# Performance work log

Measured on AMD Instinct MI355X. Metric: run time of the kernel, lower is better.

Reference implementation:

```python
import jax, jax.numpy as jnp
import numpy as np

B, T, F, H, D = 64, 256, 128, 8, 256
E = F * H          # MHA embed dim = input_dim * feat_dim = 1024
HEADS = 4
HD = E // HEADS


def setup_inputs() -> dict:
    key = jax.random.key(0)
    ks = jax.random.split(key, 12)
    def w(k, shape, fan_in):
        return (jax.random.normal(k, shape, jnp.float32) / np.float32(np.sqrt(fan_in)))
    z = lambda *s: jnp.zeros(s, jnp.float32)
    return {
        "x": jax.random.normal(ks[0], (B, T, F), jnp.float32),
        # input_attn MLP: Linear(F, F//4) -> GELU -> Linear(F//4, F) -> Sigmoid
        "attn_w1": w(ks[1], (F, F // 4), F), "attn_b1": z(F // 4),
        "attn_w2": w(ks[2], (F // 4, F), F // 4), "attn_b2": z(F),
        # bank of F tiny GRUs (input=1, hidden=H), stacked along feature axis
        "W_ih": w(ks[3], (F, 3 * H), 1),        # input weight per feature (input size 1)
        "W_hh": w(ks[4], (F, 3 * H, H), H),
        "b_ih": z(F, 3 * H), "b_hh": z(F, 3 * H),
        # MultiheadAttention(E, 4 heads)
        "in_proj_w": w(ks[5], (E, 3 * E), E), "in_proj_b": z(3 * E),
        "mha_out_w": w(ks[6], (E, E), E), "mha_out_b": z(E),
        # out_proj: Linear(E, D)
        "outp_w": w(ks[7], (E, D), E), "outp_b": z(D),
        # FFN: Linear(D, 2D) -> GELU -> Linear(2D, D)
        "ffn_w1": w(ks[8], (D, 2 * D), D), "ffn_b1": z(2 * D),
        "ffn_w2": w(ks[9], (2 * D, D), 2 * D), "ffn_b2": z(D),
    }


def _forward(x, attn_w1, attn_b1, attn_w2, attn_b2,
             W_ih, W_hh, b_ih, b_hh,
             in_proj_w, in_proj_b, mha_out_w, mha_out_b,
             outp_w, outp_b, ffn_w1, ffn_b1, ffn_w2, ffn_b2):
    gelu = lambda v: jax.nn.gelu(v, approximate=False)
    bs, ts, _ = x.shape
    # feature gating (dropout layers are identity in eval mode)
    input_attn = jax.nn.sigmoid(gelu(x @ attn_w1 + attn_b1) @ attn_w2 + attn_b2)  # [B,T,F]
    xg = x * input_attn

    # fused bank of F independent GRUs (input size 1, hidden H), scanned over time
    def step(h, xt):  # h: [B,F,H], xt: [B,F]
        gi = xt[..., None] * W_ih + b_ih                       # [B,F,3H]
        gh = jnp.einsum('bfh,fgh->bfg', h, W_hh) + b_hh        # [B,F,3H]
        ir, iz, inn = jnp.split(gi, 3, axis=-1)
        hr, hz, hn = jnp.split(gh, 3, axis=-1)
        r = jax.nn.sigmoid(ir + hr)
        zg = jax.nn.sigmoid(iz + hz)
        n = jnp.tanh(inn + r * hn)
        h_new = (1.0 - zg) * n + zg * h
        return h_new, h_new

    h0 = jnp.zeros((bs, F, H), x.dtype)
    _, ys = jax.lax.scan(step, h0, jnp.moveaxis(xg, 1, 0))     # ys: [T,B,F,H]
    out = jnp.moveaxis(ys, 0, 1).reshape(bs, ts, E)            # [B,T,E]

    # self-attention (eval: no dropout)
    qkv = out @ in_proj_w + in_proj_b                          # [B,T,3E]
    q, k, v = jnp.split(qkv, 3, axis=-1)
    hsplit = lambda t: t.reshape(bs, ts, HEADS, HD)
    q, k, v = hsplit(q), hsplit(k), hsplit(v)
    scores = jnp.einsum('bqhd,bkhd->bhqk', q, k) / np.float32(np.sqrt(HD))
    attn = jax.nn.softmax(scores, axis=-1)
    ctx = jnp.einsum('bhqk,bkhd->bqhd', attn, v).reshape(bs, ts, E)
    mha_out = ctx @ mha_out_w + mha_out_b

    h1 = mha_out @ outp_w + outp_b                             # [B,T,D]
    ffn = gelu(h1 @ ffn_w1 + ffn_b1) @ ffn_w2 + ffn_b2
    y = h1 + ffn
    feature_importance = input_attn.sum(-1)                    # [B,T]
    return y, feature_importance, input_attn


def reference(x, attn_w1, attn_b1, attn_w2, attn_b2,
              W_ih, W_hh, b_ih, b_hh,
              in_proj_w, in_proj_b, mha_out_w, mha_out_b,
              outp_w, outp_b, ffn_w1, ffn_b1, ffn_w2, ffn_b2):
    return _forward(x, attn_w1, attn_b1, attn_w2, attn_b2,
                    W_ih, W_hh, b_ih, b_hh,
                    in_proj_w, in_proj_b, mha_out_w, mha_out_b,
                    outp_w, outp_b, ffn_w1, ffn_b1, ffn_w2, ffn_b2)
```

## Files before the change

kernel.cpp:

```cpp
#include <hip/hip_runtime.h>
#include <hip/hip_bf16.h>
#include <math.h>

#define B_  64
#define T_  256
#define F_  128
#define H_  8
#define E_  1024
#define NH_ 4
#define HD_ 256
#define D_  256

#define OFF_Y_  0L
#define OFF_FI_ 4194304L
#define OFF_IA_ 4210688L

typedef unsigned short u16;
typedef unsigned int   u32;
typedef short bf16x8 __attribute__((ext_vector_type(8)));
typedef float f32x4  __attribute__((ext_vector_type(4)));

__device__ __forceinline__ float bf2f(u16 u) {
  union { u32 u; float f; } x; x.u = ((u32)u) << 16; return x.f;
}
__device__ __forceinline__ u16 f2bf(float f) {
  union { float f; u32 u; } x; x.f = f;
  u32 r = (x.u + 0x7fffu + ((x.u >> 16) & 1u)) >> 16;
  return (u16)r;
}
__device__ __forceinline__ float gelu_exact(float v) {
  return 0.5f * v * (1.f + erff(v * 0.70710678118654752f));
}
__device__ __forceinline__ float sigmoidf_(float v) {
  return 1.f / (1.f + __expf(-v));
}
__device__ __forceinline__ float ldv(const void* p, long i, bool isf) {
  return isf ? ((const float*)p)[i] : bf2f(((const u16*)p)[i]);
}
__device__ __forceinline__ void stv(void* p, long i, float v, bool isf) {
  if (isf) ((float*)p)[i] = v;
  else ((u16*)p)[i] = f2bf(v);
}
__device__ __forceinline__ void gld16(void* lds, const void* g) {
  __builtin_amdgcn_global_load_lds(
      (const __attribute__((address_space(1))) u32*)g,
      (__attribute__((address_space(3))) u32*)lds, 16, 0, 0);
}
#define MFMA_ __builtin_amdgcn_mfma_f32_16x16x32_bf16

__global__ void detect_dtype(const u16* __restrict__ x, u32* __restrict__ flag) {
  if (threadIdx.x == 0 && blockIdx.x == 0) {
    int good = 0;
    for (int i = 0; i < 512; ++i) {
      u16 v = x[i];
      int e = (v >> 7) & 0xFF;
      if (v == 0 || (e >= 100 && e <= 140)) ++good;
    }
    *flag = (good >= 450) ? 0u : 1u;
  }
}

__device__ __forceinline__ void do_transpose(const void* __restrict__ in,
                                             u16* __restrict__ out, int R, int C,
                                             int bx, int by, bool isf,
                                             float (*t)[33], int tid) {
  const int tx = tid & 31, ty0 = tid >> 5;
  const int c0 = bx * 32, r0 = by * 32;
  for (int i = ty0; i < 32; i += 8)
    t[i][tx] = ldv(in, (long)(r0 + i) * C + c0 + tx, isf);
  __syncthreads();
  for (int i = ty0; i < 32; i += 8)
    out[(long)(c0 + i) * R + r0 + tx] = f2bf(t[tx][i]);
}

__global__ __launch_bounds__(256)
void uberprep(const void* __restrict__ x,
              const void* __restrict__ w1, const void* __restrict__ b1,
              const void* __restrict__ w2, const void* __restrict__ b2,
              const void* __restrict__ ipw, const void* __restrict__ mhw,
              const void* __restrict__ opw, const void* __restrict__ f1w,
              const void* __restrict__ f2w,
              const void* __restrict__ ipb, const void* __restrict__ mhb,
              const void* __restrict__ opb, const void* __restrict__ f1b,
              const void* __restrict__ f2b,
              const u32* __restrict__ flag,
              u16* __restrict__ xg,
              u16* __restrict__ wtI, u16* __restrict__ wtM, u16* __restrict__ wtO,
              u16* __restrict__ wtF1, u16* __restrict__ wtF2,
              u16* __restrict__ biasa, void* __restrict__ dout) {
  const bool isf = (*flag != 0);
  const int bid = blockIdx.x;
  const int tid = threadIdx.x;
  __shared__ float xr[2][F_];
  __shared__ float hid4[2][4][32];
  __shared__ float hid[2][32];
  __shared__ float red[4];
  __shared__ float tt[32][33];
  if (bid < 8192) {
    const int sub = tid >> 7, t7 = tid & 127;
    const long row = (long)bid * 2 + sub;
    float xv = ldv(x, row * F_ + t7, isf);
    xr[sub][t7] = xv;
    __syncthreads();
    {
      const int g = t7 & 31, part = t7 >> 5;
      const int f0 = part * 32;
      float s = 0.f;
      #pragma unroll 8
      for (int f = 0; f < 32; ++f)
        s += xr[sub][f0 + f] * ldv(w1, (long)(f0 + f) * 32 + g, isf);
      hid4[sub][part][g] = s;
    }
    __syncthreads();
    if (t7 < 32)
      hid[sub][t7] = gelu_exact(ldv(b1, t7, isf) + hid4[sub][0][t7] + hid4[sub][1][t7]
                                + hid4[sub][2][t7] + hid4[sub][3][t7]);
    __syncthreads();
    float s = ldv(b2, t7, isf);
    #pragma unroll 8
    for (int j = 0; j < 32; ++j) s += hid[sub][j] * ldv(w2, j * F_ + t7, isf);
    float ia = sigmoidf_(s);
    stv(dout, OFF_IA_ + row * F_ + t7, ia, isf);
    xg[row * F_ + t7] = f2bf(ia * xv);
    float v = ia;
    for (int o = 32; o > 0; o >>= 1) v += __shfl_down(v, o);
    if ((tid & 63) == 0) red[tid >> 6] = v;
    __syncthreads();
    if (t7 == 0) stv(dout, OFF_FI_ + row, red[sub * 2] + red[sub * 2 + 1], isf);
  } else if (bid < 11264) {
    const int r = bid - 8192;
    do_transpose(ipw, wtI, 1024, 3072, r % 96, r / 96, isf, tt, tid);
  } else if (bid < 12288) {
    const int r = bid - 11264;
    do_transpose(mhw, wtM, 1024, 1024, r % 32, r / 32, isf, tt, tid);
  } else if (bid < 12544) {
    const int r = bid - 12288;
    do_transpose(opw, wtO, 1024, 256, r % 8, r / 8, isf, tt, tid);
  } else if (bid < 12672) {
    const int r = bid - 12544;
    do_transpose(f1w, wtF1, 256, 512, r % 16, r / 16, isf, tt, tid);
  } else if (bid < 12800) {
    const int r = bid - 12672;
    do_transpose(f2w, wtF2, 512, 256, r % 8, r / 8, isf, tt, tid);
  } else {
    const int i = (bid - 12800) * 256 + tid;
    if (i < 5120) {
      const void* s; long off;
      if (i < 3072)      { s = ipb; off = i; }
      else if (i < 4096) { s = mhb; off = i - 3072; }
      else if (i < 4352) { s = opb; off = i - 4096; }
      else if (i < 4864) { s = f1b; off = i - 4352; }
      else               { s = f2b; off = i - 4864; }
      biasa[i] = f2bf(ldv(s, off, isf));
    }
  }
}

__global__ __launch_bounds__(256)
void gru_scan4(const u16* __restrict__ xg, const void* __restrict__ W_ih,
               const void* __restrict__ W_hh, const void* __restrict__ b_ih,
               const void* __restrict__ b_hh, const u32* __restrict__ flag,
               u16* __restrict__ gruo) {
  const bool isf = (*flag != 0);
  const int tid = threadIdx.x;
  const int ric = tid >> 3;
  const int j   = tid & 7;
  const int rec = blockIdx.x * 32 + ric;
  const int b = rec >> 7, f = rec & 127;
  __shared__ __align__(16) float hbuf[32][8];
  float whr[8], whz[8], whn[8];
  #pragma unroll
  for (int k = 0; k < 8; ++k) {
    whr[k] = ldv(W_hh, (long)f * 192 + j * 8 + k, isf);
    whz[k] = ldv(W_hh, (long)f * 192 + (8 + j) * 8 + k, isf);
    whn[k] = ldv(W_hh, (long)f * 192 + (16 + j) * 8 + k, isf);
  }
  const float wir = ldv(W_ih, f * 24 + j, isf);
  const float wiz = ldv(W_ih, f * 24 + 8 + j, isf);
  const float win = ldv(W_ih, f * 24 + 16 + j, isf);
  const float cbr = ldv(b_ih, f * 24 + j, isf) + ldv(b_hh, f * 24 + j, isf);
  const float cbz = ldv(b_ih, f * 24 + 8 + j, isf) + ldv(b_hh, f * 24 + 8 + j, isf);
  const float bin_ = ldv(b_ih, f * 24 + 16 + j, isf);
  const float bhn_ = ldv(b_hh, f * 24 + 16 + j, isf);
  float h[8];
  #pragma unroll
  for (int k = 0; k < 8; ++k) h[k] = 0.f;
  const u16* xp = xg + (long)b * T_ * F_ + f;
  u16* op = gruo + (long)b * T_ * E_ + f * 8 + j;
  float xv = bf2f(xp[0]);
  for (int t = 0; t < T_; ++t) {
    float xn = (t + 1 < T_) ? bf2f(xp[(t + 1) * F_]) : 0.f;
    float ar = fmaf(xv, wir, cbr);
    float az = fmaf(xv, wiz, cbz);
    float an = bhn_;
    #pragma unroll
    for (int k = 0; k < 8; ++k) {
      ar = fmaf(h[k], whr[k], ar);
      az = fmaf(h[k], whz[k], az);
      an = fmaf(h[k], whn[k], an);
    }
    const float r = sigmoidf_(ar);
    const float z = sigmoidf_(az);
    const float a = fmaf(r, an, fmaf(xv, win, bin_));
    const float e = __expf(2.f * a);
    const float n = 1.f - 2.f / (e + 1.f);
    const float hn = fmaf(z, h[j] - n, n);
    op[(long)t * E_] = f2bf(hn);
    hbuf[ric][j] = hn;
    f32x4 h0 = *(const f32x4*)&hbuf[ric][0];
    f32x4 h1 = *(const f32x4*)&hbuf[ric][4];
    h[0] = h0[0]; h[1] = h0[1]; h[2] = h0[2]; h[3] = h0[3];
    h[4] = h1[0]; h[5] = h1[1]; h[6] = h1[2]; h[7] = h1[3];
    xv = xn;
  }
}

template <int EPI>
__global__ __launch_bounds__(256)
void gemm_bt(const u16* __restrict__ A, int lda,
             const u16* __restrict__ Bp, int ldb,
             u16* __restrict__ Cg, int ldc,
             const u16* __restrict__ bias,
             int K, int nbm) {
  const int bm = blockIdx.x % nbm, bn = blockIdx.x / nbm;
  const int w = threadIdx.x >> 6, lane = threadIdx.x & 63;
  __shared__ __align__(16) u16 As[128 * 64];
  __shared__ __align__(16) u16 Bs[128 * 64];
  const long m0 = (long)bm * 128, n0 = (long)bn * 128;
  const int wm = w >> 1, wn = w & 1;
  const int lr8 = lane >> 3;
  const int csw = ((lane & 7) ^ (lr8 & 7)) * 8;
  f32x4 acc[4][4] = {};
  const int nk = K >> 6;
  const int lr = lane & 15, lq = lane >> 4;
  for (int kt = 0; kt < nk; ++kt) {
    const int k0 = kt << 6;
    __syncthreads();
    #pragma unroll
    for (int c = 0; c < 4; ++c) {
      const int rb = w * 32 + c * 8;
      gld16((char*)As + rb * 128, A + (m0 + rb + lr8) * (long)lda + k0 + csw);
      gld16((char*)Bs + rb * 128, Bp + (n0 + rb + lr8) * (long)ldb + k0 + csw);
    }
    __syncthreads();
    #pragma unroll
    for (int sub = 0; sub < 2; ++sub) {
      const int ch = sub * 4 + lq;
      const int cof = ((ch ^ (lr & 7)) << 3);
      bf16x8 af[4], bfv[4];
      #pragma unroll
      for (int i = 0; i < 4; ++i)
        af[i] = *(const bf16x8*)&As[(wm * 64 + i * 16 + lr) * 64 + cof];
      #pragma unroll
      for (int i = 0; i < 4; ++i)
        bfv[i] = *(const bf16x8*)&Bs[(wn * 64 + i * 16 + lr) * 64 + cof];
      #pragma unroll
      for (int i = 0; i < 4; ++i) {
        #pragma unroll
        for (int j = 0; j < 4; ++j)
          acc[i][j] = MFMA_(af[i], bfv[j], acc[i][j], 0, 0, 0);
      }
    }
  }
  const int rq = lq * 4;
  #pragma unroll
  for (int j = 0; j < 4; ++j) {
    const long col = n0 + wn * 64 + j * 16 + lr;
    const float bv = (EPI >= 1) ? bf2f(bias[col]) : 0.f;
    #pragma unroll
    for (int i = 0; i < 4; ++i) {
      const long row0 = m0 + wm * 64 + i * 16 + rq;
      #pragma unroll
      for (int q = 0; q < 4; ++q)
        Cg[(row0 + q) * (long)ldc + col] = f2bf(acc[i][j][q] + bv);
    }
  }
}

__global__ __launch_bounds__(256)
void attn_fused(const u16* __restrict__ qkv, u16* __restrict__ ctx) {
  const int z = blockIdx.y, bb = z >> 2, hh = z & 3;
  const int w = threadIdx.x >> 6, lane = threadIdx.x & 63;
  const int tid = threadIdx.x;
  const long t0 = (long)blockIdx.x * 64;
  __shared__ __align__(16) u16 P1[10240];
  __shared__ __align__(16) u16 Pl[64 * 264];
  __shared__ __align__(16) u16 Vt[256 * 40];
  const u16* qb = qkv + (long)bb * T_ * 3 * E_ + hh * HD_;
  const u16* kb = qb + E_;
  const u16* vb = qb + 2 * E_;
  const int rr = lane >> 2, cc = lane & 3;
  const int lr = lane & 15, lq = lane >> 4, lk = lq * 8;
  f32x4 acc[16] = {};
  for (int kt = 0; kt < 8; ++kt) {
    const int k0 = kt * 32;
    __syncthreads();
    gld16((char*)P1 + w * 16 * 64, qb + (t0 + w * 16 + rr) * (3L * E_) + k0 + cc * 8);
    #pragma unroll
    for (int c = 0; c < 4; ++c) {
      const int rb = w * 64 + c * 16;
      gld16((char*)P1 + 4096 + rb * 64, kb + (long)(rb + rr) * (3L * E_) + k0 + cc * 8);
    }
    __syncthreads();
    bf16x8 aq = *(const bf16x8*)&P1[(w * 16 + lr) * 32 + lk];
    #pragma unroll
    for (int nt = 0; nt < 16; ++nt) {
      bf16x8 bk = *(const bf16x8*)&P1[2048 + (nt * 16 + lr) * 32 + lk];
      acc[nt] = MFMA_(aq, bk, acc[nt], 0, 0, 0);
    }
  }
  #pragma unroll
  for (int q = 0; q < 4; ++q) {
    float mx = -3.4e38f;
    #pragma unroll
    for (int nt = 0; nt < 16; ++nt) mx = fmaxf(mx, acc[nt][q]);
    mx = fmaxf(mx, __shfl_xor(mx, 1));
    mx = fmaxf(mx, __shfl_xor(mx, 2));
    mx = fmaxf(mx, __shfl_xor(mx, 4));
    mx = fmaxf(mx, __shfl_xor(mx, 8));
    float e[16], sum = 0.f;
    #pragma unroll
    for (int nt = 0; nt < 16; ++nt) {
      e[nt] = __expf((acc[nt][q] - mx) * 0.0625f);
      sum += e[nt];
    }
    sum += __shfl_xor(sum, 1);
    sum += __shfl_xor(sum, 2);
    sum += __shfl_xor(sum, 4);
    sum += __shfl_xor(sum, 8);
    const float inv = 1.f / sum;
    const int rowl = w * 16 + lq * 4 + q;
    #pragma unroll
    for (int nt = 0; nt < 16; ++nt)
      Pl[rowl * 264 + nt * 16 + lr] = f2bf(e[nt] * inv);
  }
  f32x4 acc2[16] = {};
  for (int st = 0; st < 8; ++st) {
    const int s0 = st * 32;
    __syncthreads();
    #pragma unroll
    for (int c = 0; c < 4; ++c) {
      const int rb = w * 8 + c * 2;
      gld16((char*)P1 + rb * 512, vb + (s0 + rb + (lane >> 5)) * (3L * E_) + (lane & 31) * 8);
    }
    __syncthreads();
    u16 col[32];
    #pragma unroll
    for (int si = 0; si < 32; ++si) col[si] = P1[si * 256 + tid];
    #pragma unroll
    for (int cq = 0; cq < 4; ++cq)
      *(uint4*)&Vt[tid * 40 + cq * 8] = *(const uint4*)&col[cq * 8];
    __syncthreads();
    bf16x8 pa = *(const bf16x8*)&Pl[(w * 16 + lr) * 264 + s0 + lk];
    #pragma unroll
    for (int nt = 0; nt < 16; ++nt) {
      bf16x8 bv = *(const bf16x8*)&Vt[(nt * 16 + lr) * 40 + lk];
      acc2[nt] = MFMA_(pa, bv, acc2[nt], 0, 0, 0);
    }
  }
  const int rq = lq * 4;
  #pragma unroll
  for (int nt = 0; nt < 16; ++nt) {
    const int cold = nt * 16 + lr;
    #pragma unroll
    for (int q = 0; q < 4; ++q) {
      const long row = t0 + w * 16 + rq + q;
      ctx[((long)bb * T_ + row) * E_ + hh * HD_ + cold] = f2bf(acc2[nt][q]);
    }
  }
}

__global__ __launch_bounds__(256)
void fused_tail(const u16* __restrict__ MHA,
                const u16* __restrict__ wtO, const u16* __restrict__ wtF1,
                const u16* __restrict__ wtF2,
                const u16* __restrict__ bO, const u16* __restrict__ bF1,
                const u16* __restrict__ bF2,
                void* __restrict__ Y, const u32* __restrict__ flag) {
  const bool isf = (*flag != 0);
  const int w = threadIdx.x >> 6, lane = threadIdx.x & 63;
  const long m0 = (long)blockIdx.x * 32;
  __shared__ __align__(16) u16 Astg[32 * 64];
  __shared__ __align__(16) u16 h1s[32 * 264];
  __shared__ __align__(16) u16 ffhs[32 * 520];
  const int lr = lane & 15, lq = lane >> 4;
  const int rq = lq * 4;
  const int srow = w * 8 + (lane >> 3);
  const int csw = ((lane & 7) ^ ((lane >> 3) & 7)) * 8;
  f32x4 acc1[2][4] = {};
  for (int kt = 0; kt < 16; ++kt) {
    const int k0 = kt << 6;
    __syncthreads();
    gld16(&Astg[w * 512], MHA + (m0 + srow) * 1024L + k0 + csw);
    __syncthreads();
    #pragma unroll
    for (int kk = 0; kk < 2; ++kk) {
      const int ch = kk * 4 + lq;
      const int cof = ((ch ^ (lr & 7)) << 3);
      bf16x8 af[2];
      #pragma unroll
      for (int i = 0; i < 2; ++i)
        af[i] = *(const bf16x8*)&Astg[(i * 16 + lr) * 64 + cof];
      #pragma unroll
      for (int j = 0; j < 4; ++j) {
        const int n = w * 64 + j * 16 + lr;
        bf16x8 bfv = *(const bf16x8*)(wtO + n * 1024L + k0 + kk * 32 + lq * 8);
        #pragma unroll
        for (int i = 0; i < 2; ++i)
          acc1[i][j] = MFMA_(af[i], bfv, acc1[i][j], 0, 0, 0);
      }
    }
  }
  __syncthreads();
  #pragma unroll
  for (int j = 0; j < 4; ++j) {
    const int col = w * 64 + j * 16 + lr;
    const float bv = bf2f(bO[col]);
    #pragma unroll
    for (int i = 0; i < 2; ++i)
      #pragma unroll
      for (int q = 0; q < 4; ++q)
        h1s[(i * 16 + rq + q) * 264 + col] = f2bf(acc1[i][j][q] + bv);
  }
  __syncthreads();
  f32x4 acc2[2][8] = {};
  for (int kt = 0; kt < 8; ++kt) {
    const int k0 = kt << 5;
    bf16x8 af[2];
    #pragma unroll
    for (int i = 0; i < 2; ++i)
      af[i] = *(const bf16x8*)&h1s[(i * 16 + lr) * 264 + k0 + lq * 8];
    #pragma unroll
    for (int j = 0; j < 8; ++j) {
      const int n = w * 128 + j * 16 + lr;
      bf16x8 bfv = *(const bf16x8*)(wtF1 + n * 256L + k0 + lq * 8);
      #pragma unroll
      for (int i = 0; i < 2; ++i)
        acc2[i][j] = MFMA_(af[i], bfv, acc2[i][j], 0, 0, 0);
    }
  }
  __syncthreads();
  #pragma unroll
  for (int j = 0; j < 8; ++j) {
    const int col = w * 128 + j * 16 + lr;
    const float bv = bf2f(bF1[col]);
    #pragma unroll
    for (int i = 0; i < 2; ++i)
      #pragma unroll
      for (int q = 0; q < 4; ++q)
        ffhs[(i * 16 + rq + q) * 520 + col] = f2bf(gelu_exact(acc2[i][j][q] + bv));
  }
  __syncthreads();
  f32x4 acc3[2][4] = {};
  for (int kt = 0; kt < 16; ++kt) {
    const int k0 = kt << 5;
    bf16x8 af[2];
    #pragma unroll
    for (int i = 0; i < 2; ++i)
      af[i] = *(const bf16x8*)&ffhs[(i * 16 + lr) * 520 + k0 + lq * 8];
    #pragma unroll
    for (int j = 0; j < 4; ++j) {
      const int n = w * 64 + j * 16 + lr;
      bf16x8 bfv = *(const bf16x8*)(wtF2 + n * 512L + k0 + lq * 8);
      #pragma unroll
      for (int i = 0; i < 2; ++i)
        acc3[i][j] = MFMA_(af[i], bfv, acc3[i][j], 0, 0, 0);
    }
  }
  #pragma unroll
  for (int j = 0; j < 4; ++j) {
    const int col = w * 64 + j * 16 + lr;
    const float bv = bf2f(bF2[col]);
    #pragma unroll
    for (int i = 0; i < 2; ++i)
      #pragma unroll
      for (int q = 0; q < 4; ++q) {
        const int rl = i * 16 + rq + q;
        const float v = acc3[i][j][q] + bv + bf2f(h1s[rl * 264 + col]);
        stv(Y, (m0 + rl) * 256L + col, v, isf);
      }
  }
}

extern "C" void kernel_launch(void* const* d_in, const int* in_sizes, int n_in,
                              void* d_out, int out_size, void* d_ws, size_t ws_size,
                              hipStream_t stream) {
  (void)in_sizes; (void)n_in; (void)out_size; (void)ws_size;
  char* ws = (char*)d_ws;
  u16* BIASA = (u16*)(ws + 0);
  u32* FLAG  = (u32*)(ws + 12288);
  u16* wtI   = (u16*)(ws + 65536);
  u16* wtM   = (u16*)(ws + 6356992);
  u16* wtO   = (u16*)(ws + 8454144);
  u16* wtF1  = (u16*)(ws + 8978432);
  u16* wtF2  = (u16*)(ws + 9240576);
  u16* XG    = (u16*)(ws + 9502720);
  u16* GRUO  = (u16*)(ws + 16777216);
  u16* CTX   = GRUO;
  u16* QKV   = (u16*)(ws + 50331648);
  u16* MHA   = (u16*)(ws + 50331648);

  detect_dtype<<<1, 64, 0, stream>>>((const u16*)d_in[0], FLAG);
  uberprep<<<12820, 256, 0, stream>>>(
      d_in[0], d_in[1], d_in[2], d_in[3], d_in[4],
      d_in[9], d_in[11], d_in[13], d_in[15], d_in[17],
      d_in[10], d_in[12], d_in[14], d_in[16], d_in[18],
      FLAG, XG, wtI, wtM, wtO, wtF1, wtF2, BIASA, d_out);
  gru_scan4<<<256, 256, 0, stream>>>(XG, d_in[5], d_in[6], d_in[7], d_in[8], FLAG, GRUO);

  gemm_bt<1><<<dim3(128 * 24, 1), 256, 0, stream>>>(GRUO, 1024, wtI, 1024,
      QKV, 3072, BIASA, 1024, 128);
  attn_fused<<<dim3(4, B_ * NH_), 256, 0, stream>>>(QKV, CTX);
  gemm_bt<1><<<dim3(128 * 8, 1), 256, 0, stream>>>(CTX, 1024, wtM, 1024,
      MHA, 1024, BIASA + 3072, 1024, 128);
  fused_tail<<<512, 256, 0, stream>>>(MHA, wtO, wtF1, wtF2,
      BIASA + 4096, BIASA + 4352, BIASA + 4864, d_out, FLAG);
}
```

Baseline: 423.8 us.

## Overlap GRU scan with weight transposes and shrink GEMM K-tile to 32

Splits the gating MLP into its own kernel and merges the sequential GRU scan into the weight-transpose/bias-prep kernel, so the 256 long-running GRU blocks run concurrently with the transpose blocks instead of serially after them. The GEMM K tile is also halved from 64 to 32, with a matching LDS swizzle, which halves shared memory per block and may raise occupancy, at the cost of twice as many barrier-separated k-iterations. GRU blocks are dispatched first, so the transposes fill the remaining CUs while they run.

```diff
diff --git a/kernel.cpp b/kernel.cpp
--- a/kernel.cpp
+++ b/kernel.cpp
@@ -60,6 +60,50 @@
   }
 }
 
+__global__ __launch_bounds__(256)
+void mlp_prep(const void* __restrict__ x,
+              const void* __restrict__ w1, const void* __restrict__ b1,
+              const void* __restrict__ w2, const void* __restrict__ b2,
+              const u32* __restrict__ flag,
+              u16* __restrict__ xg, void* __restrict__ dout) {
+  const bool isf = (*flag != 0);
+  const int tid = threadIdx.x;
+  const int sub = tid >> 7, t7 = tid & 127;
+  const long row = (long)blockIdx.x * 2 + sub;
+  __shared__ float xr[2][F_];
+  __shared__ float hid4[2][4][32];
+  __shared__ float hid[2][32];
+  __shared__ float red[4];
+  float xv = ldv(x, row * F_ + t7, isf);
+  xr[sub][t7] = xv;
+  __syncthreads();
+  {
+    const int g = t7 & 31, part = t7 >> 5;
+    const int f0 = part * 32;
+    float s = 0.f;
+    #pragma unroll 8
+    for (int f = 0; f < 32; ++f)
+      s += xr[sub][f0 + f] * ldv(w1, (long)(f0 + f) * 32 + g, isf);
+    hid4[sub][part][g] = s;
+  }
+  __syncthreads();
+  if (t7 < 32)
+    hid[sub][t7] = gelu_exact(ldv(b1, t7, isf) + hid4[sub][0][t7] + hid4[sub][1][t7]
+                              + hid4[sub][2][t7] + hid4[sub][3][t7]);
+  __syncthreads();
+  float s = ldv(b2, t7, isf);
+  #pragma unroll 8
+  for (int j = 0; j < 32; ++j) s += hid[sub][j] * ldv(w2, j * F_ + t7, isf);
+  float ia = sigmoidf_(s);
+  stv(dout, OFF_IA_ + row * F_ + t7, ia, isf);
+  xg[row * F_ + t7] = f2bf(ia * xv);
+  float v = ia;
+  for (int o = 32; o > 0; o >>= 1) v += __shfl_down(v, o);
+  if ((tid & 63) == 0) red[tid >> 6] = v;
+  __syncthreads();
+  if (t7 == 0) stv(dout, OFF_FI_ + row, red[sub * 2] + red[sub * 2 + 1], isf);
+}
+
 __device__ __forceinline__ void do_transpose(const void* __restrict__ in,
                                              u16* __restrict__ out, int R, int C,
                                              int bx, int by, bool isf,
@@ -74,9 +118,9 @@
 }
 
 __global__ __launch_bounds__(256)
-void uberprep(const void* __restrict__ x,
-              const void* __restrict__ w1, const void* __restrict__ b1,
-              const void* __restrict__ w2, const void* __restrict__ b2,
+void gru_prep(const u16* __restrict__ xg, const void* __restrict__ W_ih,
+              const void* __restrict__ W_hh, const void* __restrict__ b_ih,
+              const void* __restrict__ b_hh,
               const void* __restrict__ ipw, const void* __restrict__ mhw,
               const void* __restrict__ opw, const void* __restrict__ f1w,
               const void* __restrict__ f2w,
@@ -84,66 +128,82 @@
               const void* __restrict__ opb, const void* __restrict__ f1b,
               const void* __restrict__ f2b,
               const u32* __restrict__ flag,
-              u16* __restrict__ xg,
+              u16* __restrict__ gruo,
               u16* __restrict__ wtI, u16* __restrict__ wtM, u16* __restrict__ wtO,
               u16* __restrict__ wtF1, u16* __restrict__ wtF2,
-              u16* __restrict__ biasa, void* __restrict__ dout) {
+              u16* __restrict__ biasa) {
   const bool isf = (*flag != 0);
   const int bid = blockIdx.x;
   const int tid = threadIdx.x;
-  __shared__ float xr[2][F_];
-  __shared__ float hid4[2][4][32];
-  __shared__ float hid[2][32];
-  __shared__ float red[4];
+  __shared__ __align__(16) float hbuf[32][8];
   __shared__ float tt[32][33];
-  if (bid < 8192) {
-    const int sub = tid >> 7, t7 = tid & 127;
-    const long row = (long)bid * 2 + sub;
-    float xv = ldv(x, row * F_ + t7, isf);
-    xr[sub][t7] = xv;
-    __syncthreads();
-    {
-      const int g = t7 & 31, part = t7 >> 5;
-      const int f0 = part * 32;
-      float s = 0.f;
-      #pragma unroll 8
-      for (int f = 0; f < 32; ++f)
-        s += xr[sub][f0 + f] * ldv(w1, (long)(f0 + f) * 32 + g, isf);
-      hid4[sub][part][g] = s;
-    }
-    __syncthreads();
-    if (t7 < 32)
-      hid[sub][t7] = gelu_exact(ldv(b1, t7, isf) + hid4[sub][0][t7] + hid4[sub][1][t7]
-                                + hid4[sub][2][t7] + hid4[sub][3][t7]);
-    __syncthreads();
-    float s = ldv(b2, t7, isf);
-    #pragma unroll 8
-    for (int j = 0; j < 32; ++j) s += hid[sub][j] * ldv(w2, j * F_ + t7, isf);
-    float ia = sigmoidf_(s);
-    stv(dout, OFF_IA_ + row * F_ + t7, ia, isf);
-    xg[row * F_ + t7] = f2bf(ia * xv);
-    float v = ia;
-    for (int o = 32; o > 0; o >>= 1) v += __shfl_down(v, o);
-    if ((tid & 63) == 0) red[tid >> 6] = v;
-    __syncthreads();
-    if (t7 == 0) stv(dout, OFF_FI_ + row, red[sub * 2] + red[sub * 2 + 1], isf);
-  } else if (bid < 11264) {
-    const int r = bid - 8192;
+  if (bid < 256) {
+    const int ric = tid >> 3;
+    const int j   = tid & 7;
+    const int rec = bid * 32 + ric;
+    const int b = rec >> 7, f = rec & 127;
+    float whr[8], whz[8], whn[8];
+    #pragma unroll
+    for (int k = 0; k < 8; ++k) {
+      whr[k] = ldv(W_hh, (long)f * 192 + j * 8 + k, isf);
+      whz[k] = ldv(W_hh, (long)f * 192 + (8 + j) * 8 + k, isf);
+      whn[k] = ldv(W_hh, (long)f * 192 + (16 + j) * 8 + k, isf);
+    }
+    const float wir = ldv(W_ih, f * 24 + j, isf);
+    const float wiz = ldv(W_ih, f * 24 + 8 + j, isf);
+    const float win = ldv(W_ih, f * 24 + 16 + j, isf);
+    const float cbr = ldv(b_ih, f * 24 + j, isf) + ldv(b_hh, f * 24 + j, isf);
+    const float cbz = ldv(b_ih, f * 24 + 8 + j, isf) + ldv(b_hh, f * 24 + 8 + j, isf);
+    const float bin_ = ldv(b_ih, f * 24 + 16 + j, isf);
+    const float bhn_ = ldv(b_hh, f * 24 + 16 + j, isf);
+    float h[8];
+    #pragma unroll
+    for (int k = 0; k < 8; ++k) h[k] = 0.f;
+    const u16* xp = xg + (long)b * T_ * F_ + f;
+    u16* op = gruo + (long)b * T_ * E_ + f * 8 + j;
+    float xv = bf2f(xp[0]);
+    for (int t = 0; t < T_; ++t) {
+      float xn = (t + 1 < T_) ? bf2f(xp[(t + 1) * F_]) : 0.f;
+      float ar = fmaf(xv, wir, cbr);
+      float az = fmaf(xv, wiz, cbz);
+      float an = bhn_;
+      #pragma unroll
+      for (int k = 0; k < 8; ++k) {
+        ar = fmaf(h[k], whr[k], ar);
+        az = fmaf(h[k], whz[k], az);
+        an = fmaf(h[k], whn[k], an);
+      }
+      const float r = sigmoidf_(ar);
+      const float z = sigmoidf_(az);
+      const float a = fmaf(r, an, fmaf(xv, win, bin_));
+      const float e = __expf(2.f * a);
+      const float n = 1.f - 2.f / (e + 1.f);
+      const float hn = fmaf(z, h[j] - n, n);
+      op[(long)t * E_] = f2bf(hn);
+      hbuf[ric][j] = hn;
+      f32x4 h0 = *(const f32x4*)&hbuf[ric][0];
+      f32x4 h1 = *(const f32x4*)&hbuf[ric][4];
+      h[0] = h0[0]; h[1] = h0[1]; h[2] = h0[2]; h[3] = h0[3];
+      h[4] = h1[0]; h[5] = h1[1]; h[6] = h1[2]; h[7] = h1[3];
+      xv = xn;
+    }
+  } else if (bid < 3328) {
+    const int r = bid - 256;
     do_transpose(ipw, wtI, 1024, 3072, r % 96, r / 96, isf, tt, tid);
-  } else if (bid < 12288) {
-    const int r = bid - 11264;
+  } else if (bid < 4352) {
+    const int r = bid - 3328;
     do_transpose(mhw, wtM, 1024, 1024, r % 32, r / 32, isf, tt, tid);
-  } else if (bid < 12544) {
-    const int r = bid - 12288;
+  } else if (bid < 4608) {
+    const int r = bid - 4352;
     do_transpose(opw, wtO, 1024, 256, r % 8, r / 8, isf, tt, tid);
-  } else if (bid < 12672) {
-    const int r = bid - 12544;
+  } else if (bid < 4736) {
+    const int r = bid - 4608;
     do_transpose(f1w, wtF1, 256, 512, r % 16, r / 16, isf, tt, tid);
-  } else if (bid < 12800) {
-    const int r = bid - 12672;
+  } else if (bid < 4864) {
+    const int r = bid - 4736;
     do_transpose(f2w, wtF2, 512, 256, r % 8, r / 8, isf, tt, tid);
   } else {
-    const int i = (bid - 12800) * 256 + tid;
+    const int i = (bid - 4864) * 256 + tid;
     if (i < 5120) {
       const void* s; long off;
       if (i < 3072)      { s = ipb; off = i; }
@@ -153,65 +213,6 @@
       else               { s = f2b; off = i - 4864; }
       biasa[i] = f2bf(ldv(s, off, isf));
     }
-  }
-}
-
-__global__ __launch_bounds__(256)
-void gru_scan4(const u16* __restrict__ xg, const void* __restrict__ W_ih,
-               const void* __restrict__ W_hh, const void* __restrict__ b_ih,
-               const void* __restrict__ b_hh, const u32* __restrict__ flag,
-               u16* __restrict__ gruo) {
-  const bool isf = (*flag != 0);
-  const int tid = threadIdx.x;
-  const int ric = tid >> 3;
-  const int j   = tid & 7;
-  const int rec = blockIdx.x * 32 + ric;
-  const int b = rec >> 7, f = rec & 127;
-  __shared__ __align__(16) float hbuf[32][8];
-  float whr[8], whz[8], whn[8];
-  #pragma unroll
-  for (int k = 0; k < 8; ++k) {
-    whr[k] = ldv(W_hh, (long)f * 192 + j * 8 + k, isf);
-    whz[k] = ldv(W_hh, (long)f * 192 + (8 + j) * 8 + k, isf);
-    whn[k] = ldv(W_hh, (long)f * 192 + (16 + j) * 8 + k, isf);
-  }
-  const float wir = ldv(W_ih, f * 24 + j, isf);
-  const float wiz = ldv(W_ih, f * 24 + 8 + j, isf);
-  const float win = ldv(W_ih, f * 24 + 16 + j, isf);
-  const float cbr = ldv(b_ih, f * 24 + j, isf) + ldv(b_hh, f * 24 + j, isf);
-  const float cbz = ldv(b_ih, f * 24 + 8 + j, isf) + ldv(b_hh, f * 24 + 8 + j, isf);
-  const float bin_ = ldv(b_ih, f * 24 + 16 + j, isf);
-  const float bhn_ = ldv(b_hh, f * 24 + 16 + j, isf);
-  float h[8];
-  #pragma unroll
-  for (int k = 0; k < 8; ++k) h[k] = 0.f;
-  const u16* xp = xg + (long)b * T_ * F_ + f;
-  u16* op = gruo + (long)b * T_ * E_ + f * 8 + j;
-  float xv = bf2f(xp[0]);
-  for (int t = 0; t < T_; ++t) {
-    float xn = (t + 1 < T_) ? bf2f(xp[(t + 1) * F_]) : 0.f;
-    float ar = fmaf(xv, wir, cbr);
-    float az = fmaf(xv, wiz, cbz);
-    float an = bhn_;
-    #pragma unroll
-    for (int k = 0; k < 8; ++k) {
-      ar = fmaf(h[k], whr[k], ar);
-      az = fmaf(h[k], whz[k], az);
-      an = fmaf(h[k], whn[k], an);
-    }
-    const float r = sigmoidf_(ar);
-    const float z = sigmoidf_(az);
-    const float a = fmaf(r, an, fmaf(xv, win, bin_));
-    const float e = __expf(2.f * a);
-    const float n = 1.f - 2.f / (e + 1.f);
-    const float hn = fmaf(z, h[j] - n, n);
-    op[(long)t * E_] = f2bf(hn);
-    hbuf[ric][j] = hn;
-    f32x4 h0 = *(const f32x4*)&hbuf[ric][0];
-    f32x4 h1 = *(const f32x4*)&hbuf[ric][4];
-    h[0] = h0[0]; h[1] = h0[1]; h[2] = h0[2]; h[3] = h0[3];
-    h[4] = h1[0]; h[5] = h1[1]; h[6] = h1[2]; h[7] = h1[3];
-    xv = xn;
   }
 }
 
@@ -224,42 +225,38 @@
              int K, int nbm) {
   const int bm = blockIdx.x % nbm, bn = blockIdx.x / nbm;
   const int w = threadIdx.x >> 6, lane = threadIdx.x & 63;
-  __shared__ __align__(16) u16 As[128 * 64];
-  __shared__ __align__(16) u16 Bs[128 * 64];
+  __shared__ __align__(16) u16 As[128 * 32];
+  __shared__ __align__(16) u16 Bs[128 * 32];
   const long m0 = (long)bm * 128, n0 = (long)bn * 128;
   const int wm = w >> 1, wn = w & 1;
-  const int lr8 = lane >> 3;
-  const int csw = ((lane & 7) ^ (lr8 & 7)) * 8;
+  const int rr = lane >> 2;
+  const int csw = ((lane & 3) ^ ((lane >> 3) & 3)) * 8;
   f32x4 acc[4][4] = {};
-  const int nk = K >> 6;
+  const int nk = K >> 5;
   const int lr = lane & 15, lq = lane >> 4;
+  const int co = ((lq ^ ((lr >> 1) & 3)) << 3);
   for (int kt = 0; kt < nk; ++kt) {
-    const int k0 = kt << 6;
-    __syncthreads();
-    #pragma unroll
-    for (int c = 0; c < 4; ++c) {
-      const int rb = w * 32 + c * 8;
-      gld16((char*)As + rb * 128, A + (m0 + rb + lr8) * (long)lda + k0 + csw);
-      gld16((char*)Bs + rb * 128, Bp + (n0 + rb + lr8) * (long)ldb + k0 + csw);
-    }
-    __syncthreads();
-    #pragma unroll
-    for (int sub = 0; sub < 2; ++sub) {
-      const int ch = sub * 4 + lq;
-      const int cof = ((ch ^ (lr & 7)) << 3);
-      bf16x8 af[4], bfv[4];
-      #pragma unroll
-      for (int i = 0; i < 4; ++i)
-        af[i] = *(const bf16x8*)&As[(wm * 64 + i * 16 + lr) * 64 + cof];
-      #pragma unroll
-      for (int i = 0; i < 4; ++i)
-        bfv[i] = *(const bf16x8*)&Bs[(wn * 64 + i * 16 + lr) * 64 + cof];
-      #pragma unroll
-      for (int i = 0; i < 4; ++i) {
-        #pragma unroll
-        for (int j = 0; j < 4; ++j)
-          acc[i][j] = MFMA_(af[i], bfv[j], acc[i][j], 0, 0, 0);
-      }
+    const int k0 = kt << 5;
+    __syncthreads();
+    #pragma unroll
+    for (int c = 0; c < 2; ++c) {
+      const int rb = w * 32 + c * 16;
+      gld16((char*)As + rb * 64, A + (m0 + rb + rr) * (long)lda + k0 + csw);
+      gld16((char*)Bs + rb * 64, Bp + (n0 + rb + rr) * (long)ldb + k0 + csw);
+    }
+    __syncthreads();
+    bf16x8 af[4], bfv[4];
+    #pragma unroll
+    for (int i = 0; i < 4; ++i)
+      af[i] = *(const bf16x8*)&As[(wm * 64 + i * 16 + lr) * 32 + co];
+    #pragma unroll
+    for (int i = 0; i < 4; ++i)
+      bfv[i] = *(const bf16x8*)&Bs[(wn * 64 + i * 16 + lr) * 32 + co];
+    #pragma unroll
+    for (int i = 0; i < 4; ++i) {
+      #pragma unroll
+      for (int j = 0; j < 4; ++j)
+        acc[i][j] = MFMA_(af[i], bfv[j], acc[i][j], 0, 0, 0);
     }
   }
   const int rq = lq * 4;
@@ -501,12 +498,13 @@
   u16* MHA   = (u16*)(ws + 50331648);
 
   detect_dtype<<<1, 64, 0, stream>>>((const u16*)d_in[0], FLAG);
-  uberprep<<<12820, 256, 0, stream>>>(
-      d_in[0], d_in[1], d_in[2], d_in[3], d_in[4],
+  mlp_prep<<<8192, 256, 0, stream>>>(d_in[0], d_in[1], d_in[2], d_in[3], d_in[4],
+                                     FLAG, XG, d_out);
+  gru_prep<<<4884, 256, 0, stream>>>(
+      XG, d_in[5], d_in[6], d_in[7], d_in[8],
       d_in[9], d_in[11], d_in[13], d_in[15], d_in[17],
       d_in[10], d_in[12], d_in[14], d_in[16], d_in[18],
-      FLAG, XG, wtI, wtM, wtO, wtF1, wtF2, BIASA, d_out);
-  gru_scan4<<<256, 256, 0, stream>>>(XG, d_in[5], d_in[6], d_in[7], d_in[8], FLAG, GRUO);
+      FLAG, GRUO, wtI, wtM, wtO, wtF1, wtF2, BIASA);
 
   gemm_bt<1><<<dim3(128 * 24, 1), 256, 0, stream>>>(GRUO, 1024, wtI, 1024,
       QKV, 3072, BIASA, 1024, 128);
```

Result: slower. 466.9 us (+10.2%).
